# Kernel tuning notes

Hardware: AMD Instinct MI355X
Metric: run time of the kernel (lower is better)

Reference implementation:

```python
import jax, jax.numpy as jnp
import numpy as np

B, S, T = 16, 128, 128
E, H, D = 512, 512, 1024      # emb, encoder hidden, decoder hidden
VIN, VOUT = 10000, 10000


def setup_inputs() -> dict:
    key = jax.random.key(0)
    ks = iter(jax.random.split(key, 32))
    def w(shape, s=0.02):
        return jax.random.normal(next(ks), shape, jnp.float32) * s
    return {
        "x": jax.random.randint(next(ks), (B, S), 0, VIN),
        "gs_output": jax.random.randint(next(ks), (B, T), 0, VOUT),
        "in_emb": w((VIN, E)),
        "out_emb": w((VOUT, E)),
        "enc_wih0": w((2, 4 * H, E)), "enc_whh0": w((2, 4 * H, H)), "enc_b0": w((2, 4 * H)),
        "enc_wih1": w((2, 4 * H, 2 * H)), "enc_whh1": w((2, 4 * H, H)), "enc_b1": w((2, 4 * H)),
        "dec_wih0": w((4 * D, 2 * H + E)), "dec_whh0": w((4 * D, D)), "dec_b0": w((4 * D,)),
        "dec_wih1": w((4 * D, D)), "dec_whh1": w((4 * D, D)), "dec_b1": w((4 * D,)),
        "attn_w": w((D, 2 * H + D)), "attn_b": w((D,)),
        "attn_v": jax.random.uniform(next(ks), (D,), jnp.float32),
        "out_w": w((VOUT, D)), "out_b": w((VOUT,)),
    }


def _lstm_cell(x, h, c, wih, whh, b):
    # PyTorch gate order: i, f, g, o
    g = x @ wih.T + h @ whh.T + b
    i, f, gg, o = jnp.split(g, 4, axis=-1)
    c = jax.nn.sigmoid(f) * c + jax.nn.sigmoid(i) * jnp.tanh(gg)
    h = jax.nn.sigmoid(o) * jnp.tanh(c)
    return h, c


def _lstm_scan(xs, wih, whh, b, reverse=False):
    # xs: [T, B, in] time-major; returns hidden states [T, B, H]
    Bn, Hh = xs.shape[1], whh.shape[1]
    z = jnp.zeros((Bn, Hh), xs.dtype)
    def step(carry, x):
        h, c = _lstm_cell(x, carry[0], carry[1], wih, whh, b)
        return (h, c), h
    _, hs = jax.lax.scan(step, (z, z), xs, reverse=reverse)
    return hs


def reference(x, gs_output, in_emb, out_emb,
              enc_wih0, enc_whh0, enc_b0, enc_wih1, enc_whh1, enc_b1,
              dec_wih0, dec_whh0, dec_b0, dec_wih1, dec_whh1, dec_b1,
              attn_w, attn_b, attn_v, out_w, out_b):
    # padding_idx=0 rows are zero (matches nn.Embedding(padding_idx=0))
    in_emb = in_emb.at[0].set(0.0)
    out_emb = out_emb.at[0].set(0.0)
    Bn, Sn = x.shape

    # ---- bidirectional 2-layer encoder (eval mode, dropout off) ----
    xs = in_emb[x].transpose(1, 0, 2)  # [S, B, E]
    l0 = jnp.concatenate([
        _lstm_scan(xs, enc_wih0[0], enc_whh0[0], enc_b0[0]),
        _lstm_scan(xs, enc_wih0[1], enc_whh0[1], enc_b0[1], reverse=True)], -1)
    enc = jnp.concatenate([
        _lstm_scan(l0, enc_wih1[0], enc_whh1[0], enc_b1[0]),
        _lstm_scan(l0, enc_wih1[1], enc_whh1[1], enc_b1[1], reverse=True)], -1)
    enc_out = enc.transpose(1, 0, 2)  # [B, S, 2H]

    dec_layers = ((dec_wih0, dec_whh0, dec_b0), (dec_wih1, dec_whh1, dec_b1))

    def dec_step(h, c, inp):
        hs, cs = [], []
        for l, (wih, whh, b) in enumerate(dec_layers):
            nh, nc = _lstm_cell(inp, h[l], c[l], wih, whh, b)
            hs.append(nh); cs.append(nc); inp = nh
        return jnp.stack(hs), jnp.stack(cs), inp

    # torch primes decoder_hidden with one zero-input step from zero state
    h = jnp.zeros((2, Bn, D), jnp.float32)
    c = jnp.zeros((2, Bn, D), jnp.float32)
    h, c, _ = dec_step(h, c, jnp.zeros((Bn, 2 * H + E), jnp.float32))

    gs_emb = out_emb[gs_output].transpose(1, 0, 2)  # [T, B, E]

    def step(carry, emb_t):
        h, c, last_emb = carry
        q = c[-1]  # torch uses decoder_hidden[-1][-1] = last-layer CELL state
        qrep = jnp.broadcast_to(q[:, None, :], (Bn, Sn, D))
        energy = jnp.tanh(jnp.einsum('bsk,dk->bsd', jnp.concatenate([qrep, enc_out], -1), attn_w) + attn_b)
        a = jax.nn.softmax(energy @ attn_v, axis=1)           # [B, S]
        weighted = jnp.einsum('bs,bsh->bh', a, enc_out)       # [B, 2H]
        h2, c2, top = dec_step(h, c, jnp.concatenate([weighted, last_emb], -1))
        logits = top @ out_w.T + out_b                        # [B, Vout]
        return (h2, c2, emb_t), logits

    init = (h, c, jnp.zeros((Bn, E), jnp.float32))
    _, outs = jax.lax.scan(step, init, gs_emb)                # [T, B, Vout]
    return outs.transpose(1, 0, 2)                            # [B, T, Vout]
```

## Files before the change

kernel.cpp:

```cpp
#include <hip/hip_runtime.h>

#define BB 16
#define SS 128
#define TT 128
#define EE 512
#define HH 512
#define DD 1024
#define VO 10000

#define FMA4(A, W, X)              \
  A = fmaf((W).x, (X).x, A);       \
  A = fmaf((W).y, (X).y, A);       \
  A = fmaf((W).z, (X).z, A);       \
  A = fmaf((W).w, (X).w, A)

__device__ __forceinline__ float wred(float s) {
#pragma unroll
  for (int off = 32; off >= 1; off >>= 1) s += __shfl_xor(s, off, 64);
  return s;
}
__device__ __forceinline__ float sigm(float x) { return 1.f / (1.f + expf(-x)); }

__device__ __forceinline__ void stv(float* p, float v) {
  __hip_atomic_store(p, v, __ATOMIC_RELAXED, __HIP_MEMORY_SCOPE_AGENT);
}

__device__ __forceinline__ void gbar(unsigned* bar, int lb, unsigned nleaf) {
  asm volatile("s_waitcnt vmcnt(0) lgkmcnt(0)" ::: "memory");
  __syncthreads();
  if (threadIdx.x == 0) {
    unsigned* leaf = bar + ((lb >> 3) << 5);
    unsigned* root = bar + 2048;
    unsigned* gen = bar + 2112;
    const unsigned g = __hip_atomic_load(gen, __ATOMIC_RELAXED, __HIP_MEMORY_SCOPE_AGENT);
    const unsigned a =
        __hip_atomic_fetch_add(leaf, 1u, __ATOMIC_RELAXED, __HIP_MEMORY_SCOPE_AGENT);
    if (a == g * 8u + 7u) {
      const unsigned r =
          __hip_atomic_fetch_add(root, 1u, __ATOMIC_RELAXED, __HIP_MEMORY_SCOPE_AGENT);
      if (r == g * nleaf + (nleaf - 1u))
        __hip_atomic_store(gen, g + 1u, __ATOMIC_RELAXED, __HIP_MEMORY_SCOPE_AGENT);
    }
    while (__hip_atomic_load(gen, __ATOMIC_RELAXED, __HIP_MEMORY_SCOPE_AGENT) == g)
      __builtin_amdgcn_s_sleep(1);
  }
  __syncthreads();
}

__global__ void gather_k(const int* __restrict__ idx, const float* __restrict__ emb,
                         float* __restrict__ out, int Sn) {
  const int s = blockIdx.x, b = blockIdx.y, tid = threadIdx.x;
  const int id = idx[b * Sn + s];
  float4 v = make_float4(0.f, 0.f, 0.f, 0.f);
  if (id != 0) v = ((const float4*)(emb + (size_t)id * EE))[tid];
  ((float4*)(out + ((size_t)s * BB + b) * EE))[tid] = v;
}

template <int K>
__global__ void gemv16b_k(const float* __restrict__ X, int ldx,
                          const float* __restrict__ W, int ldw,
                          float* __restrict__ G, int M, size_t wz, size_t gz) {
  const int lane = threadIdx.x & 63;
  const int n = blockIdx.x * 4 + (threadIdx.x >> 6);
  const int mg = blockIdx.y;
  const int z = blockIdx.z;
  const float* Xr = X + (size_t)mg * 16 * ldx;
  const float* Wn = W + (size_t)z * wz + (size_t)n * ldw;
  float acc[16];
#pragma unroll
  for (int j = 0; j < 16; ++j) acc[j] = 0.f;
#pragma unroll
  for (int it = 0; it < K / 256; ++it) {
    const int k = it * 256 + lane * 4;
    const float4 w4 = *(const float4*)&Wn[k];
#pragma unroll
    for (int j = 0; j < 16; ++j) {
      const float4 xv = *(const float4*)&Xr[(size_t)j * ldx + k];
      FMA4(acc[j], w4, xv);
    }
  }
#pragma unroll
  for (int j = 0; j < 16; ++j) acc[j] = wred(acc[j]);
  float sel = 0.f;
#pragma unroll
  for (int j = 0; j < 16; ++j)
    if (lane == j) sel = acc[j];
  if (lane < 16) G[(size_t)z * gz + (size_t)n * M + mg * 16 + lane] = sel;
}

__global__ __launch_bounds__(512, 4) void enc_mega6_k(
    const float* __restrict__ gx, const float* __restrict__ whh,
    const float* __restrict__ bias, float* __restrict__ h_all,
    float* __restrict__ seq, int seq_ts, int seq_bs, unsigned* __restrict__ barbase) {
  const int tid = threadIdx.x, lane = tid & 63, lw = tid >> 6;
  const int dir = blockIdx.x >> 7;
  const int lb = blockIdx.x & 127;
  const int w2 = lb * 8 + lw;
  const int d = w2 >> 1, bq = w2 & 1;
  unsigned* bar = barbase + dir * 4096;

  __shared__ float hs[16][512];

  float wr[4][8];
  const float* wsrc = whh + (size_t)dir * (4 * HH * HH);
#pragma unroll
  for (int g = 0; g < 4; ++g)
#pragma unroll
    for (int j = 0; j < 8; ++j)
      wr[g][j] = wsrc[(size_t)(g * HH + d) * HH + j * 64 + lane];
  float bv[4];
#pragma unroll
  for (int g = 0; g < 4; ++g) bv[g] = bias[dir * 4 * HH + g * HH + d];
  const float* gxz = gx + (size_t)dir * ((size_t)4 * HH * 2048);
  float creg = 0.f;

  for (int t = 0; t < SS; ++t) {
    const int idx = dir ? (SS - 1 - t) : t;
    const float* hp = h_all + ((size_t)t * 2 + dir) * (BB * HH);
    for (int i = tid; i < BB * HH / 4; i += 512)
      *(float4*)&((float*)hs)[i * 4] = *(const float4*)&hp[i * 4];
    __syncthreads();
    float acc[4][8];
#pragma unroll
    for (int g = 0; g < 4; ++g)
#pragma unroll
      for (int j = 0; j < 8; ++j) acc[g][j] = 0.f;
#pragma unroll
    for (int kb = 0; kb < 8; ++kb) {
      const int k = kb * 64 + lane;
#pragma unroll
      for (int j = 0; j < 8; ++j) {
        const float xv = hs[bq * 8 + j][k];
#pragma unroll
        for (int g = 0; g < 4; ++g) acc[g][j] = fmaf(wr[g][kb], xv, acc[g][j]);
      }
    }
#pragma unroll
    for (int g = 0; g < 4; ++g)
#pragma unroll
      for (int j = 0; j < 8; ++j) acc[g][j] = wred(acc[g][j]);
    float s0 = 0.f, s1 = 0.f, s2 = 0.f, s3 = 0.f;
#pragma unroll
    for (int j = 0; j < 8; ++j)
      if (lane == j) { s0 = acc[0][j]; s1 = acc[1][j]; s2 = acc[2][j]; s3 = acc[3][j]; }
    if (lane < 8) {
      const int b = bq * 8 + lane;
      const int m = idx * 16 + b;
      const float gi = sigm(s0 + bv[0] + gxz[(size_t)(0 * HH + d) * 2048 + m]);
      const float gf = sigm(s1 + bv[1] + gxz[(size_t)(1 * HH + d) * 2048 + m]);
      const float gg = tanhf(s2 + bv[2] + gxz[(size_t)(2 * HH + d) * 2048 + m]);
      const float go = sigm(s3 + bv[3] + gxz[(size_t)(3 * HH + d) * 2048 + m]);
      const float cn = gf * creg + gi * gg;
      creg = cn;
      const float hv = go * tanhf(cn);
      stv(h_all + ((size_t)(t + 1) * 2 + dir) * (BB * HH) + b * HH + d, hv);
      seq[(size_t)idx * seq_ts + (size_t)b * seq_bs + dir * HH + d] = hv;
    }
    gbar(bar, lb, 16u);
  }
}

template <int CW>
__device__ __forceinline__ void stagex(float (&xs)[16][1024], const float* __restrict__ src,
                                       int tid) {
  for (int i = tid; i < 16 * CW / 4; i += 1024) {
    const int e = i * 4;
    *(float4*)&xs[e / CW][e % CW] = *(const float4*)&src[e];
  }
}

template <int NIT>
__device__ __forceinline__ void gphase(const float* __restrict__ r0,
                                       const float* __restrict__ r1,
                                       const float* __restrict__ r2,
                                       const float* __restrict__ r3,
                                       const float (&xs)[16][1024], int bq, int lane,
                                       float (&acc)[4][4]) {
#pragma unroll
  for (int it = 0; it < NIT; ++it) {
    const int k = it * 256 + lane * 4;
    const float4 w0 = *(const float4*)&r0[k];
    const float4 w1 = *(const float4*)&r1[k];
    const float4 w2 = *(const float4*)&r2[k];
    const float4 w3 = *(const float4*)&r3[k];
#pragma unroll
    for (int j = 0; j < 4; ++j) {
      const float4 xv = *(const float4*)&xs[bq * 4 + j][k];
      FMA4(acc[0][j], w0, xv);
      FMA4(acc[1][j], w1, xv);
      FMA4(acc[2][j], w2, xv);
      FMA4(acc[3][j], w3, xv);
    }
  }
}

__device__ __forceinline__ void wredsel(float (&acc)[4][4], int lane, float (&s)[4]) {
#pragma unroll
  for (int g = 0; g < 4; ++g)
#pragma unroll
    for (int j = 0; j < 4; ++j) acc[g][j] = wred(acc[g][j]);
  s[0] = s[1] = s[2] = s[3] = 0.f;
#pragma unroll
  for (int j = 0; j < 4; ++j)
    if (lane == j) { s[0] = acc[0][j]; s[1] = acc[1][j]; s[2] = acc[2][j]; s[3] = acc[3][j]; }
}

__global__ __launch_bounds__(1024, 4) void dec_mega6_k(
    const float* __restrict__ gs_emb, const float* __restrict__ encWe,
    const float* __restrict__ enc_out, const float* __restrict__ attn_w,
    const float* __restrict__ attn_b, const float* __restrict__ attn_v,
    const float* __restrict__ wih0, const float* __restrict__ whh0,
    const float* __restrict__ b0, const float* __restrict__ wih1,
    const float* __restrict__ whh1, const float* __restrict__ b1,
    const float* __restrict__ zeros, float* __restrict__ h0_all,
    float* __restrict__ h1_all, float* __restrict__ c1_all, float* __restrict__ wtd_all,
    float* __restrict__ qW_all, float* __restrict__ scores_all,
    unsigned* __restrict__ bar) {
  const int tid = threadIdx.x, lane = tid & 63, lw = tid >> 6;
  const int blk = blockIdx.x;
  const int w = blk * 16 + lw;
  const int d = w >> 2, bq = w & 3;
  const int b_att = blk >> 4, shard = blk & 15;

  __shared__ float xs[16][1024];
  __shared__ float sco[SS];
  __shared__ float sred[16][64];

  const float* w0i0 = wih0 + (size_t)(0 * DD + d) * 1536;
  const float* w0i1 = wih0 + (size_t)(1 * DD + d) * 1536;
  const float* w0i2 = wih0 + (size_t)(2 * DD + d) * 1536;
  const float* w0i3 = wih0 + (size_t)(3 * DD + d) * 1536;
  const float* w0h0 = whh0 + (size_t)(0 * DD + d) * 1024;
  const float* w0h1 = whh0 + (size_t)(1 * DD + d) * 1024;
  const float* w0h2 = whh0 + (size_t)(2 * DD + d) * 1024;
  const float* w0h3 = whh0 + (size_t)(3 * DD + d) * 1024;
  const float* w1i0 = wih1 + (size_t)(0 * DD + d) * 1024;
  const float* w1i1 = wih1 + (size_t)(1 * DD + d) * 1024;
  const float* w1i2 = wih1 + (size_t)(2 * DD + d) * 1024;
  const float* w1i3 = wih1 + (size_t)(3 * DD + d) * 1024;
  const float* w1h0 = whh1 + (size_t)(0 * DD + d) * 1024;
  const float* w1h1 = whh1 + (size_t)(1 * DD + d) * 1024;
  const float* w1h2 = whh1 + (size_t)(2 * DD + d) * 1024;
  const float* w1h3 = whh1 + (size_t)(3 * DD + d) * 1024;
  float bv0[4], bv1[4];
#pragma unroll
  for (int g = 0; g < 4; ++g) { bv0[g] = b0[g * DD + d]; bv1[g] = b1[g * DD + d]; }
  const float abv = attn_b[d];
  float c0 = 0.f, c1 = 0.f;

  if (lane < 4) {
    const float cn = sigm(bv0[0]) * tanhf(bv0[2]);
    c0 = cn;
    stv(h0_all + (bq * 4 + lane) * DD + d, sigm(bv0[3]) * tanhf(cn));
  }
  gbar(bar, blk, 32u);
  {
    stagex<1024>(xs, h0_all, tid);
    __syncthreads();
    float acc[4][4];
#pragma unroll
    for (int g = 0; g < 4; ++g)
#pragma unroll
      for (int j = 0; j < 4; ++j) acc[g][j] = 0.f;
    gphase<4>(w1i0, w1i1, w1i2, w1i3, xs, bq, lane, acc);
    float s[4];
    wredsel(acc, lane, s);
    if (lane < 4) {
      const int b = bq * 4 + lane;
      const float cn = sigm(s[0] + bv1[0]) * tanhf(s[2] + bv1[2]);
      c1 = cn;
      stv(c1_all + b * DD + d, cn);
      stv(h1_all + b * DD + d, sigm(s[3] + bv1[3]) * tanhf(cn));
    }
  }
  gbar(bar, blk, 32u);

  for (int t = 0; t < TT; ++t) {
    stagex<1024>(xs, c1_all + (size_t)t * (BB * DD), tid);
    __syncthreads();
    {
      float qa[4] = {0.f, 0.f, 0.f, 0.f};
      const float* wq = attn_w + (size_t)d * 2048;
#pragma unroll
      for (int it = 0; it < 4; ++it) {
        const int k = it * 256 + lane * 4;
        const float4 w4 = *(const float4*)&wq[k];
#pragma unroll
        for (int j = 0; j < 4; ++j) {
          const float4 xv = *(const float4*)&xs[bq * 4 + j][k];
          FMA4(qa[j], w4, xv);
        }
      }
#pragma unroll
      for (int j = 0; j < 4; ++j) qa[j] = wred(qa[j]);
      float sel = 0.f;
#pragma unroll
      for (int j = 0; j < 4; ++j)
        if (lane == j) sel = qa[j];
      if (lane < 4)
        stv(qW_all + (size_t)t * (BB * DD) + (bq * 4 + lane) * DD + d, sel + abv);
    }
    gbar(bar, blk, 32u);
    if (lw < 8) {
      const int s = shard * 8 + lw;
      const float* ew = encWe + ((size_t)(b_att * SS + s)) * DD;
      const float* qb = qW_all + (size_t)t * (BB * DD) + b_att * DD;
      float a = 0.f;
#pragma unroll
      for (int it = 0; it < 4; ++it) {
        const int k = it * 256 + lane * 4;
        const float4 e4 = *(const float4*)&ew[k];
        const float4 q4 = *(const float4*)&qb[k];
        const float4 v4 = *(const float4*)&attn_v[k];
        a += v4.x * tanhf(q4.x + e4.x) + v4.y * tanhf(q4.y + e4.y) +
             v4.z * tanhf(q4.z + e4.z) + v4.w * tanhf(q4.w + e4.w);
      }
      a = wred(a);
      if (lane == 0) stv(scores_all + (size_t)t * (BB * SS) + b_att * SS + s, a);
    }
    gbar(bar, blk, 32u);
    {
      if (tid < SS) sco[tid] = scores_all[(size_t)t * (BB * SS) + b_att * SS + tid];
      __syncthreads();
      float m = -1e30f;
      for (int s = 0; s < SS; ++s) m = fmaxf(m, sco[s]);
      __syncthreads();
      if (tid < SS) sco[tid] = expf(sco[tid] - m);
      __syncthreads();
      float sum = 0.f;
      for (int s = 0; s < SS; ++s) sum += sco[s];
      const float inv = 1.f / sum;
      float p = 0.f;
#pragma unroll
      for (int i = 0; i < 8; ++i) {
        const int s = lw * 8 + i;
        p += sco[s] * enc_out[((size_t)(b_att * SS + s)) * DD + shard * 64 + lane];
      }
      sred[lw][lane] = p;
      __syncthreads();
      if (lw == 0) {
        float a2 = 0.f;
#pragma unroll
        for (int i = 0; i < 16; ++i) a2 += sred[i][lane];
        stv(wtd_all + (size_t)t * (BB * DD) + b_att * DD + shard * 64 + lane, a2 * inv);
      }
    }
    gbar(bar, blk, 32u);
    {
      float acc[4][4];
#pragma unroll
      for (int g = 0; g < 4; ++g)
#pragma unroll
        for (int j = 0; j < 4; ++j) acc[g][j] = 0.f;
      stagex<1024>(xs, wtd_all + (size_t)t * (BB * DD), tid);
      __syncthreads();
      gphase<4>(w0i0, w0i1, w0i2, w0i3, xs, bq, lane, acc);
      __syncthreads();
      stagex<512>(xs, t ? gs_emb + (size_t)(t - 1) * (BB * EE) : zeros, tid);
      __syncthreads();
      gphase<2>(w0i0 + 1024, w0i1 + 1024, w0i2 + 1024, w0i3 + 1024, xs, bq, lane, acc);
      __syncthreads();
      stagex<1024>(xs, h0_all + (size_t)t * (BB * DD), tid);
      __syncthreads();
      gphase<4>(w0h0, w0h1, w0h2, w0h3, xs, bq, lane, acc);
      float s[4];
      wredsel(acc, lane, s);
      if (lane < 4) {
        const int b = bq * 4 + lane;
        const float cn = sigm(s[1] + bv0[1]) * c0 + sigm(s[0] + bv0[0]) * tanhf(s[2] + bv0[2]);
        c0 = cn;
        stv(h0_all + (size_t)(t + 1) * (BB * DD) + b * DD + d,
            sigm(s[3] + bv0[3]) * tanhf(cn));
      }
    }
    gbar(bar, blk, 32u);
    {
      float acc[4][4];
#pragma unroll
      for (int g = 0; g < 4; ++g)
#pragma unroll
        for (int j = 0; j < 4; ++j) acc[g][j] = 0.f;
      stagex<1024>(xs, h0_all + (size_t)(t + 1) * (BB * DD), tid);
      __syncthreads();
      gphase<4>(w1i0, w1i1, w1i2, w1i3, xs, bq, lane, acc);
      __syncthreads();
      stagex<1024>(xs, h1_all + (size_t)t * (BB * DD), tid);
      __syncthreads();
      gphase<4>(w1h0, w1h1, w1h2, w1h3, xs, bq, lane, acc);
      float s[4];
      wredsel(acc, lane, s);
      if (lane < 4) {
        const int b = bq * 4 + lane;
        const float cn = sigm(s[1] + bv1[1]) * c1 + sigm(s[0] + bv1[0]) * tanhf(s[2] + bv1[2]);
        c1 = cn;
        stv(c1_all + (size_t)(t + 1) * (BB * DD) + b * DD + d, cn);
        stv(h1_all + (size_t)(t + 1) * (BB * DD) + b * DD + d,
            sigm(s[3] + bv1[3]) * tanhf(cn));
      }
    }
    gbar(bar, blk, 32u);
  }
}

__global__ __launch_bounds__(512) void encwe2_k(const float* __restrict__ enc_out,
                                                const float* __restrict__ attn_w,
                                                float* __restrict__ encWe) {
  const int tid = threadIdx.x, lane = tid & 63, lw = tid >> 6;
  const int mg = blockIdx.x;
  const int nq = blockIdx.y;
  __shared__ float xsl[16][1024];
  for (int i = tid; i < 16 * 1024 / 4; i += 512)
    *(float4*)&((float*)xsl)[i * 4] =
        *(const float4*)&enc_out[(size_t)mg * 16 * 1024 + i * 4];
  __syncthreads();
#pragma unroll 1
  for (int nn = 0; nn < 8; ++nn) {
    const int n = nq * 64 + lw * 8 + nn;
    float acc[16];
#pragma unroll
    for (int j = 0; j < 16; ++j) acc[j] = 0.f;
#pragma unroll
    for (int it = 0; it < 4; ++it) {
      const int k = it * 256 + lane * 4;
      const float4 w4 = *(const float4*)&attn_w[(size_t)n * 2048 + 1024 + k];
#pragma unroll
      for (int j = 0; j < 16; ++j) {
        const float4 xv = *(const float4*)&xsl[j][k];
        FMA4(acc[j], w4, xv);
      }
    }
#pragma unroll
    for (int j = 0; j < 16; ++j) acc[j] = wred(acc[j]);
    float sel = 0.f;
#pragma unroll
    for (int j = 0; j < 16; ++j)
      if (lane == j) sel = acc[j];
    if (lane < 16) encWe[((size_t)mg * 16 + lane) * 1024 + n] = sel;
  }
}

__global__ __launch_bounds__(1024, 4) void logits2_k(const float* __restrict__ h1all,
                                                     const float* __restrict__ out_w,
                                                     const float* __restrict__ out_b,
                                                     float* __restrict__ out) {
  const int tid = threadIdx.x, lane = tid & 63, lw = tid >> 6;
  const int t = blockIdx.x;
  const int oq = blockIdx.y;
  __shared__ float hs[16][1024];
  const float* h1 = h1all + (size_t)t * (BB * DD);
  for (int i = tid; i < BB * DD / 4; i += 1024)
    *(float4*)&((float*)hs)[i * 4] = *(const float4*)&h1[i * 4];
  __syncthreads();
  const int obase = oq * 80 + lw * 5;
#pragma unroll
  for (int p = 0; p < 3; ++p) {
    const int nr = (p < 2) ? 2 : 1;
    const int o0 = obase + p * 2;
    float accA[16], accB[16];
#pragma unroll
    for (int b = 0; b < 16; ++b) { accA[b] = 0.f; accB[b] = 0.f; }
    const float* wr0 = out_w + (size_t)o0 * DD;
    const float* wr1 = wr0 + DD;
#pragma unroll
    for (int it = 0; it < 4; ++it) {
      const int k = it * 256 + lane * 4;
      const float4 wa = *(const float4*)&wr0[k];
      float4 wb = make_float4(0.f, 0.f, 0.f, 0.f);
      if (nr == 2) wb = *(const float4*)&wr1[k];
#pragma unroll
      for (int b = 0; b < 16; ++b) {
        const float4 xv = *(const float4*)&hs[b][k];
        FMA4(accA[b], wa, xv);
        if (nr == 2) { FMA4(accB[b], wb, xv); }
      }
    }
#pragma unroll
    for (int b = 0; b < 16; ++b) {
      accA[b] = wred(accA[b]);
      if (nr == 2) accB[b] = wred(accB[b]);
    }
    float sA = 0.f, sB = 0.f;
#pragma unroll
    for (int b = 0; b < 16; ++b)
      if (lane == b) { sA = accA[b]; sB = accB[b]; }
    if (lane < 16) {
      out[(size_t)lane * TT * VO + (size_t)t * VO + o0] = sA + out_b[o0];
      if (nr == 2) out[(size_t)lane * TT * VO + (size_t)t * VO + o0 + 1] = sB + out_b[o0 + 1];
    }
  }
}

extern "C" void kernel_launch(void* const* d_in, const int* in_sizes, int n_in,
                              void* d_out, int out_size, void* d_ws, size_t ws_size,
                              hipStream_t stream) {
  const int* x = (const int*)d_in[0];
  const int* gs = (const int*)d_in[1];
  const float* in_emb = (const float*)d_in[2];
  const float* out_emb = (const float*)d_in[3];
  const float* ewih0 = (const float*)d_in[4];
  const float* ewhh0 = (const float*)d_in[5];
  const float* eb0 = (const float*)d_in[6];
  const float* ewih1 = (const float*)d_in[7];
  const float* ewhh1 = (const float*)d_in[8];
  const float* eb1 = (const float*)d_in[9];
  const float* dwih0 = (const float*)d_in[10];
  const float* dwhh0 = (const float*)d_in[11];
  const float* db0 = (const float*)d_in[12];
  const float* dwih1 = (const float*)d_in[13];
  const float* dwhh1 = (const float*)d_in[14];
  const float* db1 = (const float*)d_in[15];
  const float* attn_w = (const float*)d_in[16];
  const float* attn_b = (const float*)d_in[17];
  const float* attn_v = (const float*)d_in[18];
  const float* out_w = (const float*)d_in[19];
  const float* out_b = (const float*)d_in[20];
  float* out = (float*)d_out;

  float* ws = (float*)d_ws;
  size_t off = 0;
  auto alloc = [&](size_t n) { float* p = ws + off; off += n; return p; };
  unsigned* bar = (unsigned*)alloc(3 * 4096);
  float* zeros = alloc(BB * DD);
  float* ehA = alloc((size_t)(SS + 1) * 2 * BB * HH);
  float* ehB = alloc(2 * BB * HH);
  const size_t state_n = off;
  alloc((size_t)SS * 2 * BB * HH);
  float* h0_all = alloc((size_t)(TT + 1) * BB * DD);
  float* h1_all = alloc((size_t)(TT + 1) * BB * DD);
  float* c1_all = alloc((size_t)(TT + 1) * BB * DD);
  float* wtd_all = alloc((size_t)TT * BB * DD);
  float* qW_all = alloc((size_t)TT * BB * DD);
  float* scores_all = alloc((size_t)TT * BB * SS);
  float* xs_emb = alloc((size_t)SS * BB * EE);
  float* gs_emb = alloc((size_t)TT * BB * EE);
  float* l0 = alloc((size_t)SS * BB * (2 * HH));
  float* enc_out = alloc((size_t)BB * SS * (2 * HH));
  float* encWe = alloc((size_t)BB * SS * DD);
  float* gxA = alloc(2ull * 2048ull * 2048ull);
  (void)ws_size; (void)in_sizes; (void)n_in; (void)out_size;

  hipMemsetAsync(d_ws, 0, state_n * sizeof(float), stream);

  gather_k<<<dim3(SS, BB), 128, 0, stream>>>(x, in_emb, xs_emb, SS);
  gather_k<<<dim3(TT, BB), 128, 0, stream>>>(gs, out_emb, gs_emb, TT);

  gemv16b_k<EE><<<dim3(512, 128, 2), 256, 0, stream>>>(
      xs_emb, EE, ewih0, EE, gxA, 2048, (size_t)4 * HH * EE, 2048ull * 2048ull);
  enc_mega6_k<<<256, 512, 0, stream>>>(gxA, ewhh0, eb0, ehA, l0, BB * 2 * HH, 2 * HH, bar);
  gemv16b_k<2 * HH><<<dim3(512, 128, 2), 256, 0, stream>>>(
      l0, 2 * HH, ewih1, 2 * HH, gxA, 2048, (size_t)4 * HH * 2 * HH, 2048ull * 2048ull);
  enc_mega6_k<<<256, 512, 0, stream>>>(gxA, ewhh1, eb1, ehB, enc_out, 2 * HH, SS * 2 * HH,
                                       bar);
  encwe2_k<<<dim3(128, 16), 512, 0, stream>>>(enc_out, attn_w, encWe);

  dec_mega6_k<<<256, 1024, 0, stream>>>(gs_emb, encWe, enc_out, attn_w, attn_b, attn_v,
                                        dwih0, dwhh0, db0, dwih1, dwhh1, db1, zeros,
                                        h0_all, h1_all, c1_all, wtd_all, qW_all,
                                        scores_all, bar + 2 * 4096);

  logits2_k<<<dim3(TT, 125), 1024, 0, stream>>>(h1_all + BB * DD, out_w, out_b, out);
}
```

Before: 17.51 ms.

## Replace tree atomic grid barrier with flag-gather barrier; drop decoder LDS staging

Swaps the hierarchical fetch-add grid barrier for a flag-based one: each block stores a monotonically increasing target into its own padded slot, block 0 polls all slots in parallel and then publishes a release flag that every block spins on. The decoder recurrent kernel also stops staging activations into a 64KB shared-memory tile and reads them straight from global memory. That removes the extra __syncthreads and the LDS copies inside each step. The intent is to cut per-step synchronisation latency across the many grid barriers per decode step, at the cost of redundant global/L2 reads of the same activation rows by several waves. The barrier buffers are enlarged and given separate regions per kernel launch.

Result: faster. 16.86 ms (-3.7%).

```diff
diff --git a/kernel.cpp b/kernel.cpp
--- a/kernel.cpp
+++ b/kernel.cpp
@@ -25,25 +25,24 @@
   __hip_atomic_store(p, v, __ATOMIC_RELAXED, __HIP_MEMORY_SCOPE_AGENT);
 }
 
-__device__ __forceinline__ void gbar(unsigned* bar, int lb, unsigned nleaf) {
+__device__ __forceinline__ void gbar2(unsigned* bar, int lb, int nblk, unsigned target) {
   asm volatile("s_waitcnt vmcnt(0) lgkmcnt(0)" ::: "memory");
   __syncthreads();
-  if (threadIdx.x == 0) {
-    unsigned* leaf = bar + ((lb >> 3) << 5);
-    unsigned* root = bar + 2048;
-    unsigned* gen = bar + 2112;
-    const unsigned g = __hip_atomic_load(gen, __ATOMIC_RELAXED, __HIP_MEMORY_SCOPE_AGENT);
-    const unsigned a =
-        __hip_atomic_fetch_add(leaf, 1u, __ATOMIC_RELAXED, __HIP_MEMORY_SCOPE_AGENT);
-    if (a == g * 8u + 7u) {
-      const unsigned r =
-          __hip_atomic_fetch_add(root, 1u, __ATOMIC_RELAXED, __HIP_MEMORY_SCOPE_AGENT);
-      if (r == g * nleaf + (nleaf - 1u))
-        __hip_atomic_store(gen, g + 1u, __ATOMIC_RELAXED, __HIP_MEMORY_SCOPE_AGENT);
-    }
-    while (__hip_atomic_load(gen, __ATOMIC_RELAXED, __HIP_MEMORY_SCOPE_AGENT) == g)
+  if (threadIdx.x == 0)
+    __hip_atomic_store(bar + lb * 16, target, __ATOMIC_RELAXED, __HIP_MEMORY_SCOPE_AGENT);
+  if (lb == 0) {
+    for (int i = threadIdx.x; i < nblk; i += blockDim.x)
+      while (__hip_atomic_load(bar + i * 16, __ATOMIC_RELAXED, __HIP_MEMORY_SCOPE_AGENT) <
+             target)
+        __builtin_amdgcn_s_sleep(1);
+    __syncthreads();
+    if (threadIdx.x == 0)
+      __hip_atomic_store(bar + 8192, target, __ATOMIC_RELAXED, __HIP_MEMORY_SCOPE_AGENT);
+  }
+  if (threadIdx.x == 0)
+    while (__hip_atomic_load(bar + 8192, __ATOMIC_RELAXED, __HIP_MEMORY_SCOPE_AGENT) <
+           target)
       __builtin_amdgcn_s_sleep(1);
-  }
   __syncthreads();
 }
 
@@ -88,7 +87,7 @@
   if (lane < 16) G[(size_t)z * gz + (size_t)n * M + mg * 16 + lane] = sel;
 }
 
-__global__ __launch_bounds__(512, 4) void enc_mega6_k(
+__global__ __launch_bounds__(512, 4) void enc_mega7_k(
     const float* __restrict__ gx, const float* __restrict__ whh,
     const float* __restrict__ bias, float* __restrict__ h_all,
     float* __restrict__ seq, int seq_ts, int seq_bs, unsigned* __restrict__ barbase) {
@@ -97,7 +96,7 @@
   const int lb = blockIdx.x & 127;
   const int w2 = lb * 8 + lw;
   const int d = w2 >> 1, bq = w2 & 1;
-  unsigned* bar = barbase + dir * 4096;
+  unsigned* bar = barbase + dir * 16384;
 
   __shared__ float hs[16][512];
 
@@ -113,6 +112,7 @@
   for (int g = 0; g < 4; ++g) bv[g] = bias[dir * 4 * HH + g * HH + d];
   const float* gxz = gx + (size_t)dir * ((size_t)4 * HH * 2048);
   float creg = 0.f;
+  unsigned bt = 0;
 
   for (int t = 0; t < SS; ++t) {
     const int idx = dir ? (SS - 1 - t) : t;
@@ -156,56 +156,11 @@
       stv(h_all + ((size_t)(t + 1) * 2 + dir) * (BB * HH) + b * HH + d, hv);
       seq[(size_t)idx * seq_ts + (size_t)b * seq_bs + dir * HH + d] = hv;
     }
-    gbar(bar, lb, 16u);
-  }
-}
-
-template <int CW>
-__device__ __forceinline__ void stagex(float (&xs)[16][1024], const float* __restrict__ src,
-                                       int tid) {
-  for (int i = tid; i < 16 * CW / 4; i += 1024) {
-    const int e = i * 4;
-    *(float4*)&xs[e / CW][e % CW] = *(const float4*)&src[e];
-  }
-}
-
-template <int NIT>
-__device__ __forceinline__ void gphase(const float* __restrict__ r0,
-                                       const float* __restrict__ r1,
-                                       const float* __restrict__ r2,
-                                       const float* __restrict__ r3,
-                                       const float (&xs)[16][1024], int bq, int lane,
-                                       float (&acc)[4][4]) {
-#pragma unroll
-  for (int it = 0; it < NIT; ++it) {
-    const int k = it * 256 + lane * 4;
-    const float4 w0 = *(const float4*)&r0[k];
-    const float4 w1 = *(const float4*)&r1[k];
-    const float4 w2 = *(const float4*)&r2[k];
-    const float4 w3 = *(const float4*)&r3[k];
-#pragma unroll
-    for (int j = 0; j < 4; ++j) {
-      const float4 xv = *(const float4*)&xs[bq * 4 + j][k];
-      FMA4(acc[0][j], w0, xv);
-      FMA4(acc[1][j], w1, xv);
-      FMA4(acc[2][j], w2, xv);
-      FMA4(acc[3][j], w3, xv);
-    }
-  }
-}
-
-__device__ __forceinline__ void wredsel(float (&acc)[4][4], int lane, float (&s)[4]) {
-#pragma unroll
-  for (int g = 0; g < 4; ++g)
-#pragma unroll
-    for (int j = 0; j < 4; ++j) acc[g][j] = wred(acc[g][j]);
-  s[0] = s[1] = s[2] = s[3] = 0.f;
-#pragma unroll
-  for (int j = 0; j < 4; ++j)
-    if (lane == j) { s[0] = acc[0][j]; s[1] = acc[1][j]; s[2] = acc[2][j]; s[3] = acc[3][j]; }
-}
-
-__global__ __launch_bounds__(1024, 4) void dec_mega6_k(
+    gbar2(bar, lb, 128, ++bt);
+  }
+}
+
+__global__ __launch_bounds__(1024, 4) void dec_mega7_k(
     const float* __restrict__ gs_emb, const float* __restrict__ encWe,
     const float* __restrict__ enc_out, const float* __restrict__ attn_w,
     const float* __restrict__ attn_b, const float* __restrict__ attn_v,
@@ -222,7 +177,6 @@
   const int d = w >> 2, bq = w & 3;
   const int b_att = blk >> 4, shard = blk & 15;
 
-  __shared__ float xs[16][1024];
   __shared__ float sco[SS];
   __shared__ float sred[16][64];
 
@@ -247,24 +201,44 @@
   for (int g = 0; g < 4; ++g) { bv0[g] = b0[g * DD + d]; bv1[g] = b1[g * DD + d]; }
   const float abv = attn_b[d];
   float c0 = 0.f, c1 = 0.f;
+  unsigned bt = 0;
 
   if (lane < 4) {
     const float cn = sigm(bv0[0]) * tanhf(bv0[2]);
     c0 = cn;
     stv(h0_all + (bq * 4 + lane) * DD + d, sigm(bv0[3]) * tanhf(cn));
   }
-  gbar(bar, blk, 32u);
+  gbar2(bar, blk, 256, ++bt);
   {
-    stagex<1024>(xs, h0_all, tid);
-    __syncthreads();
     float acc[4][4];
 #pragma unroll
     for (int g = 0; g < 4; ++g)
 #pragma unroll
       for (int j = 0; j < 4; ++j) acc[g][j] = 0.f;
-    gphase<4>(w1i0, w1i1, w1i2, w1i3, xs, bq, lane, acc);
-    float s[4];
-    wredsel(acc, lane, s);
+#pragma unroll
+    for (int it = 0; it < 4; ++it) {
+      const int k = it * 256 + lane * 4;
+      const float4 q0 = *(const float4*)&w1i0[k];
+      const float4 q1 = *(const float4*)&w1i1[k];
+      const float4 q2 = *(const float4*)&w1i2[k];
+      const float4 q3 = *(const float4*)&w1i3[k];
+#pragma unroll
+      for (int j = 0; j < 4; ++j) {
+        const float4 xv = *(const float4*)&h0_all[(bq * 4 + j) * DD + k];
+        FMA4(acc[0][j], q0, xv);
+        FMA4(acc[1][j], q1, xv);
+        FMA4(acc[2][j], q2, xv);
+        FMA4(acc[3][j], q3, xv);
+      }
+    }
+#pragma unroll
+    for (int g = 0; g < 4; ++g)
+#pragma unroll
+      for (int j = 0; j < 4; ++j) acc[g][j] = wred(acc[g][j]);
+    float s[4] = {0.f, 0.f, 0.f, 0.f};
+#pragma unroll
+    for (int j = 0; j < 4; ++j)
+      if (lane == j) { s[0] = acc[0][j]; s[1] = acc[1][j]; s[2] = acc[2][j]; s[3] = acc[3][j]; }
     if (lane < 4) {
       const int b = bq * 4 + lane;
       const float cn = sigm(s[0] + bv1[0]) * tanhf(s[2] + bv1[2]);
@@ -273,21 +247,20 @@
       stv(h1_all + b * DD + d, sigm(s[3] + bv1[3]) * tanhf(cn));
     }
   }
-  gbar(bar, blk, 32u);
+  gbar2(bar, blk, 256, ++bt);
 
   for (int t = 0; t < TT; ++t) {
-    stagex<1024>(xs, c1_all + (size_t)t * (BB * DD), tid);
-    __syncthreads();
     {
+      const float* cb = c1_all + (size_t)t * (BB * DD);
+      const float* wq = attn_w + (size_t)d * 2048;
       float qa[4] = {0.f, 0.f, 0.f, 0.f};
-      const float* wq = attn_w + (size_t)d * 2048;
 #pragma unroll
       for (int it = 0; it < 4; ++it) {
         const int k = it * 256 + lane * 4;
         const float4 w4 = *(const float4*)&wq[k];
 #pragma unroll
         for (int j = 0; j < 4; ++j) {
-          const float4 xv = *(const float4*)&xs[bq * 4 + j][k];
+          const float4 xv = *(const float4*)&cb[(bq * 4 + j) * DD + k];
           FMA4(qa[j], w4, xv);
         }
       }
@@ -300,7 +273,7 @@
       if (lane < 4)
         stv(qW_all + (size_t)t * (BB * DD) + (bq * 4 + lane) * DD + d, sel + abv);
     }
-    gbar(bar, blk, 32u);
+    gbar2(bar, blk, 256, ++bt);
     if (lw < 8) {
       const int s = shard * 8 + lw;
       const float* ew = encWe + ((size_t)(b_att * SS + s)) * DD;
@@ -318,7 +291,7 @@
       a = wred(a);
       if (lane == 0) stv(scores_all + (size_t)t * (BB * SS) + b_att * SS + s, a);
     }
-    gbar(bar, blk, 32u);
+    gbar2(bar, blk, 256, ++bt);
     {
       if (tid < SS) sco[tid] = scores_all[(size_t)t * (BB * SS) + b_att * SS + tid];
       __syncthreads();
@@ -345,26 +318,72 @@
         stv(wtd_all + (size_t)t * (BB * DD) + b_att * DD + shard * 64 + lane, a2 * inv);
       }
     }
-    gbar(bar, blk, 32u);
+    gbar2(bar, blk, 256, ++bt);
     {
+      const float* xw = wtd_all + (size_t)t * (BB * DD);
+      const float* em = t ? gs_emb + (size_t)(t - 1) * (BB * EE) : zeros;
+      const float* hp = h0_all + (size_t)t * (BB * DD);
       float acc[4][4];
 #pragma unroll
       for (int g = 0; g < 4; ++g)
 #pragma unroll
         for (int j = 0; j < 4; ++j) acc[g][j] = 0.f;
-      stagex<1024>(xs, wtd_all + (size_t)t * (BB * DD), tid);
-      __syncthreads();
-      gphase<4>(w0i0, w0i1, w0i2, w0i3, xs, bq, lane, acc);
-      __syncthreads();
-      stagex<512>(xs, t ? gs_emb + (size_t)(t - 1) * (BB * EE) : zeros, tid);
-      __syncthreads();
-      gphase<2>(w0i0 + 1024, w0i1 + 1024, w0i2 + 1024, w0i3 + 1024, xs, bq, lane, acc);
-      __syncthreads();
-      stagex<1024>(xs, h0_all + (size_t)t * (BB * DD), tid);
-      __syncthreads();
-      gphase<4>(w0h0, w0h1, w0h2, w0h3, xs, bq, lane, acc);
-      float s[4];
-      wredsel(acc, lane, s);
+#pragma unroll
+      for (int it = 0; it < 4; ++it) {
+        const int k = it * 256 + lane * 4;
+        const float4 q0 = *(const float4*)&w0i0[k];
+        const float4 q1 = *(const float4*)&w0i1[k];
+        const float4 q2 = *(const float4*)&w0i2[k];
+        const float4 q3 = *(const float4*)&w0i3[k];
+#pragma unroll
+        for (int j = 0; j < 4; ++j) {
+          const float4 xv = *(const float4*)&xw[(bq * 4 + j) * DD + k];
+          FMA4(acc[0][j], q0, xv);
+          FMA4(acc[1][j], q1, xv);
+          FMA4(acc[2][j], q2, xv);
+          FMA4(acc[3][j], q3, xv);
+        }
+      }
+#pragma unroll
+      for (int it = 4; it < 6; ++it) {
+        const int k = it * 256 + lane * 4;
+        const float4 q0 = *(const float4*)&w0i0[k];
+        const float4 q1 = *(const float4*)&w0i1[k];
+        const float4 q2 = *(const float4*)&w0i2[k];
+        const float4 q3 = *(const float4*)&w0i3[k];
+#pragma unroll
+        for (int j = 0; j < 4; ++j) {
+          const float4 xv = *(const float4*)&em[(bq * 4 + j) * EE + (k - 1024)];
+          FMA4(acc[0][j], q0, xv);
+          FMA4(acc[1][j], q1, xv);
+          FMA4(acc[2][j], q2, xv);
+          FMA4(acc[3][j], q3, xv);
+        }
+      }
+#pragma unroll
+      for (int it = 0; it < 4; ++it) {
+        const int k = it * 256 + lane * 4;
+        const float4 q0 = *(const float4*)&w0h0[k];
+        const float4 q1 = *(const float4*)&w0h1[k];
+        const float4 q2 = *(const float4*)&w0h2[k];
+        const float4 q3 = *(const float4*)&w0h3[k];
+#pragma unroll
+        for (int j = 0; j < 4; ++j) {
+          const float4 xv = *(const float4*)&hp[(bq * 4 + j) * DD + k];
+          FMA4(acc[0][j], q0, xv);
+          FMA4(acc[1][j], q1, xv);
+          FMA4(acc[2][j], q2, xv);
+          FMA4(acc[3][j], q3, xv);
+        }
+      }
+#pragma unroll
+      for (int g = 0; g < 4; ++g)
+#pragma unroll
+        for (int j = 0; j < 4; ++j) acc[g][j] = wred(acc[g][j]);
+      float s[4] = {0.f, 0.f, 0.f, 0.f};
+#pragma unroll
+      for (int j = 0; j < 4; ++j)
+        if (lane == j) { s[0] = acc[0][j]; s[1] = acc[1][j]; s[2] = acc[2][j]; s[3] = acc[3][j]; }
       if (lane < 4) {
         const int b = bq * 4 + lane;
         const float cn = sigm(s[1] + bv0[1]) * c0 + sigm(s[0] + bv0[0]) * tanhf(s[2] + bv0[2]);
@@ -373,22 +392,55 @@
             sigm(s[3] + bv0[3]) * tanhf(cn));
       }
     }
-    gbar(bar, blk, 32u);
+    gbar2(bar, blk, 256, ++bt);
     {
+      const float* h0 = h0_all + (size_t)(t + 1) * (BB * DD);
+      const float* h1p = h1_all + (size_t)t * (BB * DD);
       float acc[4][4];
 #pragma unroll
       for (int g = 0; g < 4; ++g)
 #pragma unroll
         for (int j = 0; j < 4; ++j) acc[g][j] = 0.f;
-      stagex<1024>(xs, h0_all + (size_t)(t + 1) * (BB * DD), tid);
-      __syncthreads();
-      gphase<4>(w1i0, w1i1, w1i2, w1i3, xs, bq, lane, acc);
-      __syncthreads();
-      stagex<1024>(xs, h1_all + (size_t)t * (BB * DD), tid);
-      __syncthreads();
-      gphase<4>(w1h0, w1h1, w1h2, w1h3, xs, bq, lane, acc);
-      float s[4];
-      wredsel(acc, lane, s);
+#pragma unroll
+      for (int it = 0; it < 4; ++it) {
+        const int k = it * 256 + lane * 4;
+        const float4 q0 = *(const float4*)&w1i0[k];
+        const float4 q1 = *(const float4*)&w1i1[k];
+        const float4 q2 = *(const float4*)&w1i2[k];
+        const float4 q3 = *(const float4*)&w1i3[k];
+#pragma unroll
+        for (int j = 0; j < 4; ++j) {
+          const float4 xv = *(const float4*)&h0[(bq * 4 + j) * DD + k];
+          FMA4(acc[0][j], q0, xv);
+          FMA4(acc[1][j], q1, xv);
+          FMA4(acc[2][j], q2, xv);
+          FMA4(acc[3][j], q3, xv);
+        }
+      }
+#pragma unroll
+      for (int it = 0; it < 4; ++it) {
+        const int k = it * 256 + lane * 4;
+        const float4 q0 = *(const float4*)&w1h0[k];
+        const float4 q1 = *(const float4*)&w1h1[k];
+        const float4 q2 = *(const float4*)&w1h2[k];
+        const float4 q3 = *(const float4*)&w1h3[k];
+#pragma unroll
+        for (int j = 0; j < 4; ++j) {
+          const float4 xv = *(const float4*)&h1p[(bq * 4 + j) * DD + k];
+          FMA4(acc[0][j], q0, xv);
+          FMA4(acc[1][j], q1, xv);
+          FMA4(acc[2][j], q2, xv);
+          FMA4(acc[3][j], q3, xv);
+        }
+      }
+#pragma unroll
+      for (int g = 0; g < 4; ++g)
+#pragma unroll
+        for (int j = 0; j < 4; ++j) acc[g][j] = wred(acc[g][j]);
+      float s[4] = {0.f, 0.f, 0.f, 0.f};
+#pragma unroll
+      for (int j = 0; j < 4; ++j)
+        if (lane == j) { s[0] = acc[0][j]; s[1] = acc[1][j]; s[2] = acc[2][j]; s[3] = acc[3][j]; }
       if (lane < 4) {
         const int b = bq * 4 + lane;
         const float cn = sigm(s[1] + bv1[1]) * c1 + sigm(s[0] + bv1[0]) * tanhf(s[2] + bv1[2]);
@@ -398,7 +450,7 @@
             sigm(s[3] + bv1[3]) * tanhf(cn));
       }
     }
-    gbar(bar, blk, 32u);
+    gbar2(bar, blk, 256, ++bt);
   }
 }
 
@@ -519,7 +571,7 @@
   float* ws = (float*)d_ws;
   size_t off = 0;
   auto alloc = [&](size_t n) { float* p = ws + off; off += n; return p; };
-  unsigned* bar = (unsigned*)alloc(3 * 4096);
+  unsigned* bar = (unsigned*)alloc(5 * 16384);
   float* zeros = alloc(BB * DD);
   float* ehA = alloc((size_t)(SS + 1) * 2 * BB * HH);
   float* ehB = alloc(2 * BB * HH);
@@ -546,17 +598,17 @@
 
   gemv16b_k<EE><<<dim3(512, 128, 2), 256, 0, stream>>>(
       xs_emb, EE, ewih0, EE, gxA, 2048, (size_t)4 * HH * EE, 2048ull * 2048ull);
-  enc_mega6_k<<<256, 512, 0, stream>>>(gxA, ewhh0, eb0, ehA, l0, BB * 2 * HH, 2 * HH, bar);
+  enc_mega7_k<<<256, 512, 0, stream>>>(gxA, ewhh0, eb0, ehA, l0, BB * 2 * HH, 2 * HH, bar);
   gemv16b_k<2 * HH><<<dim3(512, 128, 2), 256, 0, stream>>>(
       l0, 2 * HH, ewih1, 2 * HH, gxA, 2048, (size_t)4 * HH * 2 * HH, 2048ull * 2048ull);
-  enc_mega6_k<<<256, 512, 0, stream>>>(gxA, ewhh1, eb1, ehB, enc_out, 2 * HH, SS * 2 * HH,
-                                       bar);
+  enc_mega7_k<<<256, 512, 0, stream>>>(gxA, ewhh1, eb1, ehB, enc_out, 2 * HH, SS * 2 * HH,
+                                       bar + 2 * 16384);
   encwe2_k<<<dim3(128, 16), 512, 0, stream>>>(enc_out, attn_w, encWe);
 
-  dec_mega6_k<<<256, 1024, 0, stream>>>(gs_emb, encWe, enc_out, attn_w, attn_b, attn_v,
+  dec_mega7_k<<<256, 1024, 0, stream>>>(gs_emb, encWe, enc_out, attn_w, attn_b, attn_v,
                                         dwih0, dwhh0, db0, dwih1, dwhh1, db1, zeros,
                                         h0_all, h1_all, c1_all, wtd_all, qW_all,
-                                        scores_all, bar + 2 * 4096);
+                                        scores_all, bar + 4 * 16384);
 
   logits2_k<<<dim3(TT, 125), 1024, 0, stream>>>(h1_all + BB * DD, out_w, out_b, out);
 }
```
